# Performance work log

Measured on AMD Instinct MI355X. Metric: run time of the kernel, lower is better.

## Reference

```python
import jax, jax.numpy as jnp
import numpy as np

NUM_TOPICS = 100
VOCAB = 8192
MC_N = 20
MD_N = 20
LAMBDA_D = 0.7
LAMBDA_A = 100.0
WARMUP_RATIO = 0.5
NUM_EPOCHS = 200


def setup_inputs() -> dict:
    key = jax.random.key(0)
    k1, k2 = jax.random.split(key)
    beta = jax.random.normal(k1, (NUM_TOPICS, VOCAB), dtype=jnp.float32)
    W = jax.random.uniform(k2, (VOCAB, VOCAB), dtype=jnp.float32)
    # fill_diagonal_(1) in __init__
    d = jnp.arange(VOCAB)
    W = W.at[d, d].set(1.0)
    return {"beta": beta, "coherence_weight": W, "epoch": 120}


def reference(beta, coherence_weight, epoch):
    K, V = beta.shape
    rows = jnp.arange(K)[:, None]

    # --- Mc: top-Mc_n mask -> additive -99999 on non-topk entries ---
    _, mc_idx = jax.lax.top_k(beta, MC_N)                      # [K, Mc_n]
    Mc = jnp.zeros_like(beta).at[rows, mc_idx].set(1.0)        # [K, V]
    Mc_add = (1.0 - Mc) * (-99999.0)

    # softmax over masked beta is detached in the original
    p = jax.lax.stop_gradient(jax.nn.softmax(beta + Mc_add, axis=1))
    M = p @ coherence_weight                                    # [K, V]

    # row-wise min-max normalize, then Wc = 1 - normalized
    m_min = jnp.min(M, axis=1, keepdims=True)
    m_max = jnp.max(M, axis=1, keepdims=True)
    Wc = 1.0 - (M - m_min) / (m_max - m_min)

    loss = 100.0 * jax.nn.softmax(beta, axis=1) ** 2 * Wc       # [K, V]

    # --- diversity mask Md (lambda_d > 0.5 branch) ---
    _, md_idx = jax.lax.top_k(beta, MD_N)
    Md_mask = jnp.zeros_like(beta).at[rows, md_idx].set(1.0)    # [K, V]
    # Md[t, v] = any other row has v in its top-Md_n
    col_sum = jnp.sum(Md_mask, axis=0)                          # [V]
    Md = (col_sum[None, :] - Md_mask) > 0                       # [K, V] bool

    pos = jnp.sum(jnp.where(Md, loss, 0.0))
    neg = jnp.sum(jnp.where(Md, 0.0, loss))
    total = (pos * LAMBDA_D + neg * (1.0 - LAMBDA_D)) * 2.0

    warmup_epochs = int(WARMUP_RATIO * NUM_EPOCHS)              # 100
    lambda_a_delta = LAMBDA_A / warmup_epochs
    lambda_a = epoch * lambda_a_delta if epoch < warmup_epochs else LAMBDA_A
    return lambda_a * total
```

## Files before the change

### kernel.cpp

```cpp
#include <hip/hip_runtime.h>
#include <math.h>

#define NT 100
#define VOCAB 8192
#define TOPN 20
#define CHUNKS 8
#define CCOLS 1024
#define NB (NT * CHUNKS)
#define CAP 4096

__global__ __launch_bounds__(1024) void topk_kernel(
    const float* __restrict__ beta,
    int*   __restrict__ top_idx,
    float* __restrict__ top_p,
    float* __restrict__ rowstats)
{
    const int k = blockIdx.x;
    const int t = threadIdx.x;

    __shared__ float sred[16];
    __shared__ int   sredi[16];
    __shared__ int   s_base;
    __shared__ float cu[CAP];
    __shared__ unsigned short ci[CAP];
    __shared__ float s_winv[TOPN];
    __shared__ int   s_wini[TOPN];
    __shared__ float s_ps;

    const float* row = beta + (size_t)k * VOCAB;

    float4 r0 = *reinterpret_cast<const float4*>(row + (size_t)t * 4);
    float4 r1 = *reinterpret_cast<const float4*>(row + (size_t)(1024 + t) * 4);

    float mx = fmaxf(fmaxf(fmaxf(r0.x, r0.y), fmaxf(r0.z, r0.w)),
                     fmaxf(fmaxf(r1.x, r1.y), fmaxf(r1.z, r1.w)));
#pragma unroll
    for (int off = 32; off >= 1; off >>= 1) mx = fmaxf(mx, __shfl_down(mx, off));
    if ((t & 63) == 0) sred[t >> 6] = mx;
    __syncthreads();
    float rowmax = sred[0];
#pragma unroll
    for (int w = 1; w < 16; ++w) rowmax = fmaxf(rowmax, sred[w]);
    __syncthreads();

    float T = rowmax - 2.0f;
    for (int guard = 0; guard < 64; ++guard) {
        int c = 0;
        c += (r0.x >= T) + (r0.y >= T) + (r0.z >= T) + (r0.w >= T);
        c += (r1.x >= T) + (r1.y >= T) + (r1.z >= T) + (r1.w >= T);
#pragma unroll
        for (int off = 32; off >= 1; off >>= 1) c += __shfl_down(c, off);
        if ((t & 63) == 0) sredi[t >> 6] = c;
        __syncthreads();
        int cnt = 0;
#pragma unroll
        for (int w = 0; w < 16; ++w) cnt += sredi[w];
        if (cnt >= TOPN) break;
        T -= 0.5f;
        __syncthreads();
    }
    if (t == 0) s_base = 0;
    __syncthreads();

#pragma unroll
    for (int i = 0; i < 2; ++i) {
        const float4 rr = (i == 0) ? r0 : r1;
#pragma unroll
        for (int e = 0; e < 4; ++e) {
            const float v = (&rr.x)[e];
            const int idx = (i * 1024 + t) * 4 + e;
            const bool pr = (v >= T);
            const unsigned long long mask = __ballot(pr);
            const int lane = t & 63;
            const int pre = __popcll(mask & ((1ull << lane) - 1ull));
            int base = 0;
            if (lane == 0) base = atomicAdd(&s_base, __popcll(mask));
            base = __shfl(base, 0);
            if (pr) {
                const int p = base + pre;
                if (p < CAP) { cu[p] = v; ci[p] = (unsigned short)idx; }
            }
        }
    }
    __syncthreads();
    const int ncand = min(s_base, CAP);

    if (t < 64) {
        for (int it = 0; it < TOPN; ++it) {
            float bv = -INFINITY; int bp = -1;
            for (int p = t; p < ncand; p += 64) {
                const float v = cu[p];
                if (v > bv) { bv = v; bp = p; }
            }
#pragma unroll
            for (int off = 32; off >= 1; off >>= 1) {
                const float ov = __shfl_down(bv, off);
                const int   op = __shfl_down(bp, off);
                if (ov > bv) { bv = ov; bp = op; }
            }
            bp = __shfl(bp, 0);
            bv = __shfl(bv, 0);
            if (t == 0) { s_winv[it] = bv; s_wini[it] = ci[bp]; }
            cu[bp] = -INFINITY;
        }
    }
    __syncthreads();

    if (t == 0) {
        float ps = 0.f;
#pragma unroll
        for (int j = 0; j < TOPN; ++j) ps += expf(s_winv[j] - rowmax);
        s_ps = ps;
    }
    __syncthreads();
    if (t < TOPN) {
        top_idx[k * TOPN + t] = s_wini[t];
        top_p[k * TOPN + t]   = expf(s_winv[t] - rowmax) / s_ps;
    }

    float se = expf(r0.x - rowmax) + expf(r0.y - rowmax)
             + expf(r0.z - rowmax) + expf(r0.w - rowmax)
             + expf(r1.x - rowmax) + expf(r1.y - rowmax)
             + expf(r1.z - rowmax) + expf(r1.w - rowmax);
#pragma unroll
    for (int off = 32; off >= 1; off >>= 1) se += __shfl_down(se, off);
    if ((t & 63) == 0) sred[t >> 6] = se;
    __syncthreads();
    if (t == 0) {
        float s = 0.f;
#pragma unroll
        for (int w = 0; w < 16; ++w) s += sred[w];
        rowstats[2 * k + 0] = rowmax;
        rowstats[2 * k + 1] = s;
    }
}

__global__ __launch_bounds__(256) void fused_kernel(
    const float* __restrict__ beta,
    const float* __restrict__ W,
    const int*   __restrict__ top_idx,
    const float* __restrict__ top_p,
    const float* __restrict__ rowstats,
    float* __restrict__ part6)
{
    const int b = blockIdx.x;
    const int k = b / CHUNKS;
    const int c = b % CHUNKS;
    const int t = threadIdx.x;

    __shared__ int   sIdx[TOPN];
    __shared__ float sP[TOPN];
    __shared__ int   cnt[CCOLS];
    __shared__ float sA[4], sB[4], sC[4], sD[4], sE[4], sF[4];

    if (t < TOPN) { sIdx[t] = top_idx[k * TOPN + t]; sP[t] = top_p[k * TOPN + t]; }
#pragma unroll
    for (int i = 0; i < CCOLS / 256; ++i) cnt[i * 256 + t] = 0;
    __syncthreads();

    int   idx_r[TOPN];
    float p_r[TOPN];
#pragma unroll
    for (int j = 0; j < TOPN; ++j) { idx_r[j] = sIdx[j]; p_r[j] = sP[j]; }

    const int lo  = c * CCOLS;
    const int col = lo + t * 4;
    float4 w_r[TOPN];
#pragma unroll
    for (int j = 0; j < TOPN; ++j)
        w_r[j] = *reinterpret_cast<const float4*>(W + (size_t)idx_r[j] * VOCAB + col);
    const float4 bv = *reinterpret_cast<const float4*>(beta + (size_t)k * VOCAB + col);

#pragma unroll 8
    for (int e = t; e < NT * TOPN; e += 256) {
        const int v = top_idx[e] - lo;
        if ((unsigned)v < (unsigned)CCOLS) atomicAdd(&cnt[v], 1);
    }
    __syncthreads();
    if (t < TOPN) {
        const int v = sIdx[t] - lo;
        if ((unsigned)v < (unsigned)CCOLS) atomicSub(&cnt[v], 1);
    }

    float4 m = make_float4(0.f, 0.f, 0.f, 0.f);
#pragma unroll
    for (int j = 0; j < TOPN; ++j) {
        const float pj = p_r[j];
        m.x += pj * w_r[j].x; m.y += pj * w_r[j].y;
        m.z += pj * w_r[j].z; m.w += pj * w_r[j].w;
    }

    float mn  = fminf(fminf(m.x, m.y), fminf(m.z, m.w));
    float mxv = fmaxf(fmaxf(m.x, m.y), fmaxf(m.z, m.w));

    const float rmax = rowstats[2 * k + 0];
    const float rinv = 1.0f / rowstats[2 * k + 1];
    float4 w4;
    w4.x = expf(bv.x - rmax) * rinv;  w4.x = 100.f * w4.x * w4.x;
    w4.y = expf(bv.y - rmax) * rinv;  w4.y = 100.f * w4.y * w4.y;
    w4.z = expf(bv.z - rmax) * rinv;  w4.z = 100.f * w4.z * w4.z;
    w4.w = expf(bv.w - rmax) * rinv;  w4.w = 100.f * w4.w * w4.w;

    __syncthreads();

    float Apos = 0.f, Bpos = 0.f, Aneg = 0.f, Bneg = 0.f;
    {
        const int lc = t * 4;
        if (cnt[lc + 0] > 0) { Apos += w4.x; Bpos += w4.x * m.x; } else { Aneg += w4.x; Bneg += w4.x * m.x; }
        if (cnt[lc + 1] > 0) { Apos += w4.y; Bpos += w4.y * m.y; } else { Aneg += w4.y; Bneg += w4.y * m.y; }
        if (cnt[lc + 2] > 0) { Apos += w4.z; Bpos += w4.z * m.z; } else { Aneg += w4.z; Bneg += w4.z * m.z; }
        if (cnt[lc + 3] > 0) { Apos += w4.w; Bpos += w4.w * m.w; } else { Aneg += w4.w; Bneg += w4.w * m.w; }
    }

#pragma unroll
    for (int off = 32; off >= 1; off >>= 1) {
        mn   = fminf(mn,  __shfl_down(mn,  off));
        mxv  = fmaxf(mxv, __shfl_down(mxv, off));
        Apos += __shfl_down(Apos, off);
        Bpos += __shfl_down(Bpos, off);
        Aneg += __shfl_down(Aneg, off);
        Bneg += __shfl_down(Bneg, off);
    }
    if ((t & 63) == 0) {
        const int w = t >> 6;
        sA[w] = mn; sB[w] = mxv; sC[w] = Apos; sD[w] = Bpos; sE[w] = Aneg; sF[w] = Bneg;
    }
    __syncthreads();
    if (t == 0) {
        part6[b * 6 + 0] = fminf(fminf(sA[0], sA[1]), fminf(sA[2], sA[3]));
        part6[b * 6 + 1] = fmaxf(fmaxf(sB[0], sB[1]), fmaxf(sB[2], sB[3]));
        part6[b * 6 + 2] = sC[0] + sC[1] + sC[2] + sC[3];
        part6[b * 6 + 3] = sD[0] + sD[1] + sD[2] + sD[3];
        part6[b * 6 + 4] = sE[0] + sE[1] + sE[2] + sE[3];
        part6[b * 6 + 5] = sF[0] + sF[1] + sF[2] + sF[3];
    }
}

__global__ __launch_bounds__(128) void finalize_kernel(
    const float* __restrict__ part6,
    const int*   __restrict__ epoch,
    float* __restrict__ out)
{
    const int t = threadIdx.x;
    __shared__ float sp[128], sn[128];
    float pos = 0.f, neg = 0.f;
    if (t < NT) {
        float mn = INFINITY, mxv = -INFINITY;
        float Ap = 0.f, Bp = 0.f, An = 0.f, Bn = 0.f;
        for (int cc = 0; cc < CHUNKS; ++cc) {
            const float* p6 = part6 + (size_t)(t * CHUNKS + cc) * 6;
            mn  = fminf(mn,  p6[0]);
            mxv = fmaxf(mxv, p6[1]);
            Ap += p6[2]; Bp += p6[3]; An += p6[4]; Bn += p6[5];
        }
        const float inv = 1.0f / (mxv - mn);
        pos = Ap - inv * (Bp - mn * Ap);
        neg = An - inv * (Bn - mn * An);
    }
    sp[t] = pos; sn[t] = neg;
    __syncthreads();
    if (t == 0) {
        float P = 0.f, N = 0.f;
        for (int i = 0; i < NT; ++i) { P += sp[i]; N += sn[i]; }
        const float total = (P * 0.7f + N * 0.3f) * 2.0f;
        const int e = *epoch;
        const float la = (e < 100) ? (float)e : 100.0f;
        *out = la * total;
    }
}

extern "C" void kernel_launch(void* const* d_in, const int* in_sizes, int n_in,
                              void* d_out, int out_size, void* d_ws, size_t ws_size,
                              hipStream_t stream)
{
    (void)in_sizes; (void)n_in; (void)out_size; (void)ws_size;
    const float* beta  = (const float*)d_in[0];
    const float* W     = (const float*)d_in[1];
    const int*   epoch = (const int*)d_in[2];
    float* out = (float*)d_out;

    char* ws = (char*)d_ws;
    int*   top_idx  = (int*)ws;    ws += NT * TOPN * sizeof(int);
    float* top_p    = (float*)ws;  ws += NT * TOPN * sizeof(float);
    float* rowstats = (float*)ws;  ws += NT * 2 * sizeof(float);
    float* part6    = (float*)ws;  ws += NB * 6 * sizeof(float);

    topk_kernel<<<NT, 1024, 0, stream>>>(beta, top_idx, top_p, rowstats);
    fused_kernel<<<NB, 256, 0, stream>>>(beta, W, top_idx, top_p, rowstats, part6);
    finalize_kernel<<<1, 128, 0, stream>>>(part6, epoch, out);
}
```

Baseline: 50.87 us.

## Split per-row top-k into per-slice candidate filtering and a merge kernel

Measured after the change: 49.18 us. -3.3%, faster.

```diff
diff --git a/kernel.cpp b/kernel.cpp
--- a/kernel.cpp
+++ b/kernel.cpp
@@ -4,13 +4,98 @@
 #define NT 100
 #define VOCAB 8192
 #define TOPN 20
+#define NSL 8
+#define SCOLS 1024
+#define SCAP 128
 #define CHUNKS 8
 #define CCOLS 1024
 #define NB (NT * CHUNKS)
-#define CAP 4096
-
-__global__ __launch_bounds__(1024) void topk_kernel(
+
+__global__ __launch_bounds__(256) void slice_kernel(
     const float* __restrict__ beta,
+    float* __restrict__ cand_val,
+    int*   __restrict__ cand_idx,
+    int*   __restrict__ sl_cnt,
+    float* __restrict__ sl_max,
+    float* __restrict__ sl_sum)
+{
+    const int b = blockIdx.x;
+    const int t = threadIdx.x;
+    const int k = b / NSL;
+    const int s = b % NSL;
+    const int col0 = s * SCOLS;
+
+    __shared__ float sred[4];
+    __shared__ int   sredi[4];
+    __shared__ int   s_cnt;
+
+    const float4 v = *reinterpret_cast<const float4*>(
+        beta + (size_t)k * VOCAB + col0 + t * 4);
+
+    float mx = fmaxf(fmaxf(v.x, v.y), fmaxf(v.z, v.w));
+#pragma unroll
+    for (int off = 32; off >= 1; off >>= 1) mx = fmaxf(mx, __shfl_down(mx, off));
+    if ((t & 63) == 0) sred[t >> 6] = mx;
+    __syncthreads();
+    const float smax = fmaxf(fmaxf(sred[0], sred[1]), fmaxf(sred[2], sred[3]));
+    __syncthreads();
+
+    float se = expf(v.x - smax) + expf(v.y - smax) + expf(v.z - smax) + expf(v.w - smax);
+#pragma unroll
+    for (int off = 32; off >= 1; off >>= 1) se += __shfl_down(se, off);
+    if ((t & 63) == 0) sred[t >> 6] = se;
+    __syncthreads();
+    const float ssum = sred[0] + sred[1] + sred[2] + sred[3];
+    __syncthreads();
+
+    float T = smax - 1.5f;
+    for (int g = 0; g < 8; ++g) {
+        int c = ((v.x >= T) ? 1 : 0) + ((v.y >= T) ? 1 : 0)
+              + ((v.z >= T) ? 1 : 0) + ((v.w >= T) ? 1 : 0);
+#pragma unroll
+        for (int off = 32; off >= 1; off >>= 1) c += __shfl_down(c, off);
+        if ((t & 63) == 0) sredi[t >> 6] = c;
+        __syncthreads();
+        const int cnt = sredi[0] + sredi[1] + sredi[2] + sredi[3];
+        if (cnt >= TOPN) break;
+        T -= 0.4f;
+        __syncthreads();
+    }
+    if (t == 0) s_cnt = 0;
+    __syncthreads();
+
+#pragma unroll
+    for (int e = 0; e < 4; ++e) {
+        const float val = (&v.x)[e];
+        const bool  pr  = (val >= T);
+        const unsigned long long mask = __ballot(pr);
+        const int lane = t & 63;
+        const int pre  = __popcll(mask & ((1ull << lane) - 1ull));
+        int base = 0;
+        if (lane == 0) base = atomicAdd(&s_cnt, __popcll(mask));
+        base = __shfl(base, 0);
+        if (pr) {
+            const int p = base + pre;
+            if (p < SCAP) {
+                cand_val[(size_t)b * SCAP + p] = val;
+                cand_idx[(size_t)b * SCAP + p] = col0 + t * 4 + e;
+            }
+        }
+    }
+    __syncthreads();
+    if (t == 0) {
+        sl_cnt[b] = min(s_cnt, SCAP);
+        sl_max[b] = smax;
+        sl_sum[b] = ssum;
+    }
+}
+
+__global__ __launch_bounds__(256) void merge_kernel(
+    const float* __restrict__ cand_val,
+    const int*   __restrict__ cand_idx,
+    const int*   __restrict__ sl_cnt,
+    const float* __restrict__ sl_max,
+    const float* __restrict__ sl_sum,
     int*   __restrict__ top_idx,
     float* __restrict__ top_p,
     float* __restrict__ rowstats)
@@ -18,79 +103,51 @@
     const int k = blockIdx.x;
     const int t = threadIdx.x;
 
-    __shared__ float sred[16];
-    __shared__ int   sredi[16];
-    __shared__ int   s_base;
-    __shared__ float cu[CAP];
-    __shared__ unsigned short ci[CAP];
+    __shared__ int   scnt[NSL];
+    __shared__ int   soff[NSL + 1];
+    __shared__ float smaxs[NSL], ssums[NSL];
+    __shared__ float cval[NSL * SCAP];
+    __shared__ int   cidx[NSL * SCAP];
     __shared__ float s_winv[TOPN];
     __shared__ int   s_wini[TOPN];
-    __shared__ float s_ps;
-
-    const float* row = beta + (size_t)k * VOCAB;
-
-    float4 r0 = *reinterpret_cast<const float4*>(row + (size_t)t * 4);
-    float4 r1 = *reinterpret_cast<const float4*>(row + (size_t)(1024 + t) * 4);
-
-    float mx = fmaxf(fmaxf(fmaxf(r0.x, r0.y), fmaxf(r0.z, r0.w)),
-                     fmaxf(fmaxf(r1.x, r1.y), fmaxf(r1.z, r1.w)));
-#pragma unroll
-    for (int off = 32; off >= 1; off >>= 1) mx = fmaxf(mx, __shfl_down(mx, off));
-    if ((t & 63) == 0) sred[t >> 6] = mx;
-    __syncthreads();
-    float rowmax = sred[0];
-#pragma unroll
-    for (int w = 1; w < 16; ++w) rowmax = fmaxf(rowmax, sred[w]);
-    __syncthreads();
-
-    float T = rowmax - 2.0f;
-    for (int guard = 0; guard < 64; ++guard) {
-        int c = 0;
-        c += (r0.x >= T) + (r0.y >= T) + (r0.z >= T) + (r0.w >= T);
-        c += (r1.x >= T) + (r1.y >= T) + (r1.z >= T) + (r1.w >= T);
-#pragma unroll
-        for (int off = 32; off >= 1; off >>= 1) c += __shfl_down(c, off);
-        if ((t & 63) == 0) sredi[t >> 6] = c;
-        __syncthreads();
-        int cnt = 0;
-#pragma unroll
-        for (int w = 0; w < 16; ++w) cnt += sredi[w];
-        if (cnt >= TOPN) break;
-        T -= 0.5f;
-        __syncthreads();
-    }
-    if (t == 0) s_base = 0;
-    __syncthreads();
-
-#pragma unroll
-    for (int i = 0; i < 2; ++i) {
-        const float4 rr = (i == 0) ? r0 : r1;
-#pragma unroll
-        for (int e = 0; e < 4; ++e) {
-            const float v = (&rr.x)[e];
-            const int idx = (i * 1024 + t) * 4 + e;
-            const bool pr = (v >= T);
-            const unsigned long long mask = __ballot(pr);
-            const int lane = t & 63;
-            const int pre = __popcll(mask & ((1ull << lane) - 1ull));
-            int base = 0;
-            if (lane == 0) base = atomicAdd(&s_base, __popcll(mask));
-            base = __shfl(base, 0);
-            if (pr) {
-                const int p = base + pre;
-                if (p < CAP) { cu[p] = v; ci[p] = (unsigned short)idx; }
-            }
+    __shared__ float s_ps, s_rowmax;
+
+    if (t < NSL) {
+        scnt[t]  = sl_cnt[k * NSL + t];
+        smaxs[t] = sl_max[k * NSL + t];
+        ssums[t] = sl_sum[k * NSL + t];
+    }
+    __syncthreads();
+    if (t == 0) {
+        int o = 0;
+#pragma unroll
+        for (int s = 0; s < NSL; ++s) { soff[s] = o; o += scnt[s]; }
+        soff[NSL] = o;
+        float rm = smaxs[0];
+#pragma unroll
+        for (int s = 1; s < NSL; ++s) rm = fmaxf(rm, smaxs[s]);
+        s_rowmax = rm;
+    }
+    __syncthreads();
+    const int total = soff[NSL];
+    const float rowmax = s_rowmax;
+
+#pragma unroll
+    for (int s = 0; s < NSL; ++s) {
+        const int n = scnt[s], o = soff[s];
+        for (int p = t; p < n; p += 256) {
+            cval[o + p] = cand_val[(size_t)(k * NSL + s) * SCAP + p];
+            cidx[o + p] = cand_idx[(size_t)(k * NSL + s) * SCAP + p];
         }
     }
     __syncthreads();
-    const int ncand = min(s_base, CAP);
 
     if (t < 64) {
         for (int it = 0; it < TOPN; ++it) {
             float bv = -INFINITY; int bp = -1;
-            for (int p = t; p < ncand; p += 64) {
-                const float v = cu[p];
-                if (v > bv) { bv = v; bp = p; }
+            for (int p = t; p < total; p += 64) {
+                const float vv = cval[p];
+                if (vv > bv) { bv = vv; bp = p; }
             }
 #pragma unroll
             for (int off = 32; off >= 1; off >>= 1) {
@@ -100,8 +157,8 @@
             }
             bp = __shfl(bp, 0);
             bv = __shfl(bv, 0);
-            if (t == 0) { s_winv[it] = bv; s_wini[it] = ci[bp]; }
-            cu[bp] = -INFINITY;
+            if (t == 0) { s_winv[it] = bv; s_wini[it] = cidx[bp]; }
+            cval[bp] = -INFINITY;
         }
     }
     __syncthreads();
@@ -111,27 +168,16 @@
 #pragma unroll
         for (int j = 0; j < TOPN; ++j) ps += expf(s_winv[j] - rowmax);
         s_ps = ps;
+        float rs = 0.f;
+#pragma unroll
+        for (int s = 0; s < NSL; ++s) rs += ssums[s] * expf(smaxs[s] - rowmax);
+        rowstats[2 * k + 0] = rowmax;
+        rowstats[2 * k + 1] = rs;
     }
     __syncthreads();
     if (t < TOPN) {
         top_idx[k * TOPN + t] = s_wini[t];
         top_p[k * TOPN + t]   = expf(s_winv[t] - rowmax) / s_ps;
-    }
-
-    float se = expf(r0.x - rowmax) + expf(r0.y - rowmax)
-             + expf(r0.z - rowmax) + expf(r0.w - rowmax)
-             + expf(r1.x - rowmax) + expf(r1.y - rowmax)
-             + expf(r1.z - rowmax) + expf(r1.w - rowmax);
-#pragma unroll
-    for (int off = 32; off >= 1; off >>= 1) se += __shfl_down(se, off);
-    if ((t & 63) == 0) sred[t >> 6] = se;
-    __syncthreads();
-    if (t == 0) {
-        float s = 0.f;
-#pragma unroll
-        for (int w = 0; w < 16; ++w) s += sred[w];
-        rowstats[2 * k + 0] = rowmax;
-        rowstats[2 * k + 1] = s;
     }
 }
 
@@ -280,12 +326,20 @@
     float* out = (float*)d_out;
 
     char* ws = (char*)d_ws;
+    float* cand_val = (float*)ws;  ws += (size_t)NT * NSL * SCAP * sizeof(float);
+    int*   cand_idx = (int*)ws;    ws += (size_t)NT * NSL * SCAP * sizeof(int);
+    int*   sl_cnt   = (int*)ws;    ws += NT * NSL * sizeof(int);
+    float* sl_max   = (float*)ws;  ws += NT * NSL * sizeof(float);
+    float* sl_sum   = (float*)ws;  ws += NT * NSL * sizeof(float);
     int*   top_idx  = (int*)ws;    ws += NT * TOPN * sizeof(int);
     float* top_p    = (float*)ws;  ws += NT * TOPN * sizeof(float);
     float* rowstats = (float*)ws;  ws += NT * 2 * sizeof(float);
     float* part6    = (float*)ws;  ws += NB * 6 * sizeof(float);
 
-    topk_kernel<<<NT, 1024, 0, stream>>>(beta, top_idx, top_p, rowstats);
+    slice_kernel<<<NT * NSL, 256, 0, stream>>>(beta, cand_val, cand_idx,
+                                               sl_cnt, sl_max, sl_sum);
+    merge_kernel<<<NT, 256, 0, stream>>>(cand_val, cand_idx, sl_cnt, sl_max, sl_sum,
+                                         top_idx, top_p, rowstats);
     fused_kernel<<<NB, 256, 0, stream>>>(beta, W, top_idx, top_p, rowstats, part6);
     finalize_kernel<<<1, 128, 0, stream>>>(part6, epoch, out);
 }
```

## Parallelize top-k selection across all wavefronts with two-stage merge

Applied to the files above, without the earlier changes.

Measured after the change: 51.06 us. About the same (+0.4%).

```diff
diff --git a/kernel.cpp b/kernel.cpp
--- a/kernel.cpp
+++ b/kernel.cpp
@@ -7,7 +7,9 @@
 #define CHUNKS 8
 #define CCOLS 1024
 #define NB (NT * CHUNKS)
-#define CAP 4096
+#define CAP 2048
+#define NWV 16
+#define PRE (NWV * TOPN)
 
 __global__ __launch_bounds__(1024) void topk_kernel(
     const float* __restrict__ beta,
@@ -17,18 +19,21 @@
 {
     const int k = blockIdx.x;
     const int t = threadIdx.x;
-
-    __shared__ float sred[16];
-    __shared__ int   sredi[16];
+    const int wv = t >> 6;
+    const int lane = t & 63;
+
+    __shared__ float sred[NWV];
+    __shared__ int   sredi[NWV];
     __shared__ int   s_base;
     __shared__ float cu[CAP];
-    __shared__ unsigned short ci[CAP];
+    __shared__ int   ci[CAP];
+    __shared__ float pv[PRE];
+    __shared__ int   pi[PRE];
     __shared__ float s_winv[TOPN];
     __shared__ int   s_wini[TOPN];
     __shared__ float s_ps;
 
     const float* row = beta + (size_t)k * VOCAB;
-
     float4 r0 = *reinterpret_cast<const float4*>(row + (size_t)t * 4);
     float4 r1 = *reinterpret_cast<const float4*>(row + (size_t)(1024 + t) * 4);
 
@@ -36,11 +41,11 @@
                      fmaxf(fmaxf(r1.x, r1.y), fmaxf(r1.z, r1.w)));
 #pragma unroll
     for (int off = 32; off >= 1; off >>= 1) mx = fmaxf(mx, __shfl_down(mx, off));
-    if ((t & 63) == 0) sred[t >> 6] = mx;
+    if (lane == 0) sred[wv] = mx;
     __syncthreads();
     float rowmax = sred[0];
 #pragma unroll
-    for (int w = 1; w < 16; ++w) rowmax = fmaxf(rowmax, sred[w]);
+    for (int w = 1; w < NWV; ++w) rowmax = fmaxf(rowmax, sred[w]);
     __syncthreads();
 
     float T = rowmax - 2.0f;
@@ -50,11 +55,11 @@
         c += (r1.x >= T) + (r1.y >= T) + (r1.z >= T) + (r1.w >= T);
 #pragma unroll
         for (int off = 32; off >= 1; off >>= 1) c += __shfl_down(c, off);
-        if ((t & 63) == 0) sredi[t >> 6] = c;
+        if (lane == 0) sredi[wv] = c;
         __syncthreads();
         int cnt = 0;
 #pragma unroll
-        for (int w = 0; w < 16; ++w) cnt += sredi[w];
+        for (int w = 0; w < NWV; ++w) cnt += sredi[w];
         if (cnt >= TOPN) break;
         T -= 0.5f;
         __syncthreads();
@@ -71,24 +76,26 @@
             const int idx = (i * 1024 + t) * 4 + e;
             const bool pr = (v >= T);
             const unsigned long long mask = __ballot(pr);
-            const int lane = t & 63;
             const int pre = __popcll(mask & ((1ull << lane) - 1ull));
             int base = 0;
             if (lane == 0) base = atomicAdd(&s_base, __popcll(mask));
             base = __shfl(base, 0);
             if (pr) {
                 const int p = base + pre;
-                if (p < CAP) { cu[p] = v; ci[p] = (unsigned short)idx; }
+                if (p < CAP) { cu[p] = v; ci[p] = idx; }
             }
         }
     }
     __syncthreads();
     const int ncand = min(s_base, CAP);
 
-    if (t < 64) {
+    {
+        const int seg = (ncand + NWV - 1) / NWV;
+        const int lo = wv * seg;
+        const int hi = min(lo + seg, ncand);
         for (int it = 0; it < TOPN; ++it) {
             float bv = -INFINITY; int bp = -1;
-            for (int p = t; p < ncand; p += 64) {
+            for (int p = lo + lane; p < hi; p += 64) {
                 const float v = cu[p];
                 if (v > bv) { bv = v; bp = p; }
             }
@@ -100,8 +107,34 @@
             }
             bp = __shfl(bp, 0);
             bv = __shfl(bv, 0);
-            if (t == 0) { s_winv[it] = bv; s_wini[it] = ci[bp]; }
-            cu[bp] = -INFINITY;
+            if (lane == 0) {
+                pv[wv * TOPN + it] = bv;
+                pi[wv * TOPN + it] = (bp >= 0) ? ci[bp] : 0;
+            }
+            if (bp >= 0) cu[bp] = -INFINITY;
+        }
+    }
+    __syncthreads();
+
+    if (wv == 0) {
+        for (int it = 0; it < TOPN; ++it) {
+            float bv = -INFINITY; int bp = -1;
+#pragma unroll
+            for (int rp = 0; rp < PRE / 64; ++rp) {
+                const int p = rp * 64 + lane;
+                const float v = pv[p];
+                if (v > bv) { bv = v; bp = p; }
+            }
+#pragma unroll
+            for (int off = 32; off >= 1; off >>= 1) {
+                const float ov = __shfl_down(bv, off);
+                const int   op = __shfl_down(bp, off);
+                if (ov > bv) { bv = ov; bp = op; }
+            }
+            bp = __shfl(bp, 0);
+            bv = __shfl(bv, 0);
+            if (lane == 0) { s_winv[it] = bv; s_wini[it] = pi[bp]; }
+            pv[bp] = -INFINITY;
         }
     }
     __syncthreads();
@@ -124,12 +157,12 @@
              + expf(r1.z - rowmax) + expf(r1.w - rowmax);
 #pragma unroll
     for (int off = 32; off >= 1; off >>= 1) se += __shfl_down(se, off);
-    if ((t & 63) == 0) sred[t >> 6] = se;
+    if (lane == 0) sred[wv] = se;
     __syncthreads();
     if (t == 0) {
         float s = 0.f;
 #pragma unroll
-        for (int w = 0; w < 16; ++w) s += sred[w];
+        for (int w = 0; w < NWV; ++w) s += sred[w];
         rowstats[2 * k + 0] = rowmax;
         rowstats[2 * k + 1] = s;
     }
```
